# Kernel optimization log

Hardware: AMD Instinct MI355X
Metric: run time of the kernel (lower is better)

The kernel has to match this reference:

```python
import jax, jax.numpy as jnp
import numpy as np

EPS = 1e-5
B, N, M = 4, 256, 256
L, D, INNER = 6, 64, 64  # per-layer output = D//2 = 32 channels


def conv1x1(x, W, b=None):
    # x: [batch, Cin, H, W], W: [Cout, Cin]
    y = jnp.einsum('bchw,oc->bohw', x, W)
    if b is not None:
        y = y + b[None, :, None, None]
    return y


def batchnorm(x, g, b):
    # training-mode BN (default torch .train()): batch stats over (B, H, W)
    mu = x.mean(axis=(0, 2, 3), keepdims=True)
    var = x.var(axis=(0, 2, 3), keepdims=True)
    return g[None, :, None, None] * (x - mu) * jax.lax.rsqrt(var + EPS) + b[None, :, None, None]


def prelu(x, a):
    return jnp.where(x >= 0, x, a * x)


def cross_concat(Z):
    bs = Z.shape[0] // 2
    Za, Zb = Z[:bs], Z[bs:]
    return jnp.concatenate([jnp.concatenate([Za, Zb], 1),
                            jnp.concatenate([Zb, Za], 1)], 0)


def fw_layer(Z, Wm, bm, W, g, be, a):
    # FeatureWeavingLayer with EncoderMaxPool2stream
    bs = Z.shape[0] // 2
    X = cross_concat(Z)                                   # [2bs, 2C, N, M]
    z = conv1x1(X, Wm, bm)                                # [2bs, INNER, N, M]
    za = jnp.broadcast_to(z[:bs].max(axis=2, keepdims=True), z[:bs].shape)
    zb = jnp.broadcast_to(z[bs:].max(axis=3, keepdims=True), z[bs:].shape)
    z = jnp.concatenate([jnp.concatenate([X[:bs], za], 1),
                         jnp.concatenate([X[bs:], zb], 1)], 0)
    z = conv1x1(z, W)                                     # no bias
    z = batchnorm(z, g, be)
    return prelu(z, a)


def weavenet_fwd(Za, Zb, Wm0, bm0, W0, g0, be0, Wm, bm, W, g, be, a, Wf, gf, bf):
    Zb = jnp.swapaxes(Zb, -2, -1)      # [B, C, M, N] -> [B, C, N, M]
    Z = jnp.concatenate([Za, Zb], 0)   # [2B, 1, N, M]
    bs, n, m = Za.shape[0], Za.shape[-2], Za.shape[-1]
    layers = [(Wm0, bm0, W0, g0, be0)] + [(Wm[i], bm[i], W[i], g[i], be[i]) for i in range(L - 1)]
    Z_keep = None
    for i, (Wm_, bm_, W_, g_, be_) in enumerate(layers):
        Z = fw_layer(Z, Wm_, bm_, W_, g_, be_, a)
        if i % 2 == 0:  # use_resnet
            if Z_keep is not None:
                Z = Z + Z_keep
            Z_keep = Z
    Zc = conv1x1(cross_concat(Z), Wf)  # [2B, 1, N, M]
    Zc = batchnorm(Zc, gf, bf)
    m0 = Zc[:bs].reshape(bs, n, m)
    m1 = Zc[bs:].reshape(bs, n, m)
    # HV stream aggregation
    mm = (m0 + m1) / 2.0
    agg = jnp.minimum(jax.nn.softmax(mm, axis=-1), jax.nn.softmax(mm, axis=-2))
    return agg, m0, m1


def setup_inputs() -> dict:
    key = jax.random.key(0)
    ks = jax.random.split(key, 16)
    s = 0.05
    inp = {
        'Za': jax.random.normal(ks[0], (B, 1, N, M), jnp.float32),
        'Zb': jax.random.normal(ks[1], (B, 1, M, N), jnp.float32),
        # layer 0: input_dim = sab_dim*2 = 2
        'Wm0': jax.random.normal(ks[2], (INNER, 2), jnp.float32) * s,
        'bm0': jnp.zeros((INNER,), jnp.float32),
        'W0': jax.random.normal(ks[3], (D // 2, 2 + INNER), jnp.float32) * s,
        'g0': jnp.ones((D // 2,), jnp.float32),
        'be0': jnp.zeros((D // 2,), jnp.float32),
        # layers 1..L-1: input_dim = D = 64
        'Wm': jax.random.normal(ks[4], (L - 1, INNER, D), jnp.float32) * s,
        'bm': jnp.zeros((L - 1, INNER), jnp.float32),
        'W': jax.random.normal(ks[5], (L - 1, D // 2, D + INNER), jnp.float32) * s,
        'g': jnp.ones((L - 1, D // 2), jnp.float32),
        'be': jnp.zeros((L - 1, D // 2), jnp.float32),
        # shared PReLU (single default instance shared across all layers in torch)
        'a': jnp.float32(0.25),
        # final 1x1 conv (in = D after cross_concat) + BN
        'Wf': jax.random.normal(ks[6], (1, D), jnp.float32) * s,
        'gf': jnp.ones((1,), jnp.float32),
        'bf': jnp.zeros((1,), jnp.float32),
    }
    return inp


def reference(Za, Zb, Wm0, bm0, W0, g0, be0, Wm, bm, W, g, be, a, Wf, gf, bf):
    return weavenet_fwd(Za, Zb, Wm0, bm0, W0, g0, be0, Wm, bm, W, g, be, a, Wf, gf, bf)
```

## Files before the change

kernel.cpp:

```cpp
#include <hip/hip_runtime.h>

static constexpr int NMv  = 256;
static constexpr int PIXv = 65536;

__device__ __forceinline__ unsigned fkey(float f){
    unsigned b = __float_as_uint(f);
    return (b & 0x80000000u) ? ~b : (b | 0x80000000u);
}
__device__ __forceinline__ float unfkey(unsigned k){
    unsigned b = (k & 0x80000000u) ? (k & 0x7fffffffu) : ~k;
    return __uint_as_float(b);
}

__global__ __launch_bounds__(256) void k_prep(const float* __restrict__ Za,
                                              const float* __restrict__ Zb,
                                              float* __restrict__ Z){
    __shared__ float tile[32][33];
    int b  = blockIdx.z;
    int tx = threadIdx.x, ty = threadIdx.y;
    int n0 = blockIdx.y * 32, m0 = blockIdx.x * 32;
    if (b < 4){
        const float* src = Za + (size_t)b * PIXv;
        float*       dst = Z  + (size_t)b * PIXv;
        for (int j = 0; j < 32; j += 8){
            int n = n0 + ty + j;
            dst[n * NMv + m0 + tx] = src[n * NMv + m0 + tx];
        }
    } else {
        const float* src = Zb + (size_t)(b - 4) * PIXv;
        for (int j = 0; j < 32; j += 8)
            tile[ty + j][tx] = src[(m0 + ty + j) * NMv + n0 + tx];
        __syncthreads();
        float* dst = Z + (size_t)b * PIXv;
        for (int j = 0; j < 32; j += 8)
            dst[(n0 + ty + j) * NMv + m0 + tx] = tile[tx][ty + j];
    }
}

template<int C>
__global__ __launch_bounds__(256) void k_zmax(const float* __restrict__ Z,
                                              const float* __restrict__ Wm,
                                              const float* __restrict__ bm,
                                              unsigned* __restrict__ zkey){
    constexpr int K2  = 2 * C;
    constexpr int NCH = 8;
    constexpr int NS  = (K2 * 16 + 255) / 256;
    __shared__ float Wms[K2 * 64];
    __shared__ float Xs[K2 * 68];
    int b = blockIdx.z;
    int t = threadIdx.x;
    for (int i = t; i < 64 * K2; i += 256){
        int c = i / K2, k = i % K2;
        Wms[k * 64 + c] = Wm[i];
    }
    const float* Z0 = Z + (size_t)b       * C * PIXv;
    const float* Z1 = Z + (size_t)(b ^ 4) * C * PIXv;
    int m0 = blockIdx.x * 64, n0 = blockIdx.y * NCH;
    int c0 = (t >> 3) * 2, mg = t & 7;
    float bmv0 = bm[c0], bmv1 = bm[c0 + 1];

    float4 rbuf[NS];
    auto issue = [&](int n){
        #pragma unroll
        for (int j = 0; j < NS; j++){
            int s = t + j * 256;
            if (s < K2 * 16){
                int k = s >> 4, m4 = (s & 15) * 4;
                const float* src = (k < C ? Z0 + (size_t)k * PIXv
                                          : Z1 + (size_t)(k - C) * PIXv) + n * NMv + m0 + m4;
                rbuf[j] = *(const float4*)src;
            }
        }
    };
    issue(n0);

    float mx[2][8];
    #pragma unroll
    for (int a = 0; a < 2; a++)
        #pragma unroll
        for (int j = 0; j < 8; j++) mx[a][j] = -3.4e38f;

    for (int ni = 0; ni < NCH; ni++){
        __syncthreads();
        #pragma unroll
        for (int j = 0; j < NS; j++){
            int s = t + j * 256;
            if (s < K2 * 16){
                int k = s >> 4, m4 = (s & 15) * 4;
                *(float4*)&Xs[k * 68 + m4] = rbuf[j];
            }
        }
        if (ni + 1 < NCH) issue(n0 + ni + 1);
        __syncthreads();

        float acc[2][8];
        #pragma unroll
        for (int a = 0; a < 2; a++)
            #pragma unroll
            for (int j = 0; j < 8; j++) acc[a][j] = 0.f;
        #pragma unroll 8
        for (int k = 0; k < K2; k++){
            const float2 w  = *(const float2*)&Wms[k * 64 + c0];
            const float4 x0 = *(const float4*)&Xs[k * 68 + mg * 8];
            const float4 x1 = *(const float4*)&Xs[k * 68 + mg * 8 + 4];
            acc[0][0] += w.x * x0.x; acc[0][1] += w.x * x0.y;
            acc[0][2] += w.x * x0.z; acc[0][3] += w.x * x0.w;
            acc[0][4] += w.x * x1.x; acc[0][5] += w.x * x1.y;
            acc[0][6] += w.x * x1.z; acc[0][7] += w.x * x1.w;
            acc[1][0] += w.y * x0.x; acc[1][1] += w.y * x0.y;
            acc[1][2] += w.y * x0.z; acc[1][3] += w.y * x0.w;
            acc[1][4] += w.y * x1.x; acc[1][5] += w.y * x1.y;
            acc[1][6] += w.y * x1.z; acc[1][7] += w.y * x1.w;
        }

        if (b < 4){
            #pragma unroll
            for (int a = 0; a < 2; a++)
                #pragma unroll
                for (int j = 0; j < 8; j++) mx[a][j] = fmaxf(mx[a][j], acc[a][j]);
        } else {
            int n = n0 + ni;
            #pragma unroll
            for (int a = 0; a < 2; a++){
                float v = fmaxf(fmaxf(fmaxf(acc[a][0], acc[a][1]), fmaxf(acc[a][2], acc[a][3])),
                                fmaxf(fmaxf(acc[a][4], acc[a][5]), fmaxf(acc[a][6], acc[a][7])));
                v = fmaxf(v, __shfl_xor(v, 1));
                v = fmaxf(v, __shfl_xor(v, 2));
                v = fmaxf(v, __shfl_xor(v, 4));
                if (mg == 0)
                    atomicMax(&zkey[((size_t)b * 64 + c0 + a) * NMv + n],
                              fkey(v + (a ? bmv1 : bmv0)));
            }
        }
    }
    if (b < 4){
        #pragma unroll
        for (int a = 0; a < 2; a++){
            float bmv = a ? bmv1 : bmv0;
            #pragma unroll
            for (int j = 0; j < 8; j++)
                atomicMax(&zkey[((size_t)b * 64 + c0 + a) * NMv + m0 + mg * 8 + j],
                          fkey(mx[a][j] + bmv));
        }
    }
}

__global__ __launch_bounds__(256) void k_zmaxw(const unsigned* __restrict__ zkey,
                                               const float* __restrict__ W, int Wst,
                                               float* __restrict__ zmaxW){
    int oc = blockIdx.x, b = blockIdx.y, p = threadIdx.x;
    const float* wrow = W + (size_t)oc * Wst + (Wst - 64);
    float s = 0.f;
    #pragma unroll 8
    for (int c = 0; c < 64; c++)
        s += wrow[c] * unfkey(zkey[((size_t)b * 64 + c) * NMv + p]);
    zmaxW[((size_t)b * 32 + oc) * NMv + p] = s;
}

template<int C>
__global__ __launch_bounds__(256) void k_conv(const float* __restrict__ Z,
                                              const float* __restrict__ Wl,
                                              const float* __restrict__ zmaxW,
                                              float* __restrict__ Y,
                                              float* __restrict__ pstats){
    constexpr int K2 = 2 * C;
    constexpr int KC = (K2 < 16) ? K2 : 16;
    __shared__ float Ws[K2 * 32];
    __shared__ float Xs[KC * 256];
    int b   = blockIdx.y;
    int row = blockIdx.x;
    int t   = threadIdx.x;
    int p4  = t & 63, og = t >> 6;
    for (int i = t; i < K2 * 32; i += 256){
        int k = i >> 5, oc = i & 31;
        Ws[i] = Wl[(size_t)oc * (K2 + 64) + k];
    }
    const float* Z0 = Z + ((size_t)b       * C) * PIXv + (size_t)row * NMv;
    const float* Z1 = Z + ((size_t)(b ^ 4) * C) * PIXv + (size_t)row * NMv;
    float acc[4][8];
    #pragma unroll
    for (int j = 0; j < 4; j++)
        #pragma unroll
        for (int o = 0; o < 8; o++) acc[j][o] = 0.f;

    for (int kc = 0; kc < K2; kc += KC){
        __syncthreads();
        for (int s = t; s < KC * 64; s += 256){
            int k = kc + (s >> 6), m4 = (s & 63) * 4;
            const float* src = (k < C ? Z0 + (size_t)k * PIXv
                                      : Z1 + (size_t)(k - C) * PIXv) + m4;
            *(float4*)&Xs[(s >> 6) * 256 + m4] = *(const float4*)src;
        }
        __syncthreads();
        #pragma unroll 4
        for (int kk = 0; kk < KC; kk++){
            const float4 xv = *(const float4*)&Xs[kk * 256 + p4 * 4];
            const float4 wa = *(const float4*)&Ws[(kc + kk) * 32 + og * 8];
            const float4 wb = *(const float4*)&Ws[(kc + kk) * 32 + og * 8 + 4];
            const float xx[4] = {xv.x, xv.y, xv.z, xv.w};
            const float ww[8] = {wa.x, wa.y, wa.z, wa.w, wb.x, wb.y, wb.z, wb.w};
            #pragma unroll
            for (int j = 0; j < 4; j++)
                #pragma unroll
                for (int o = 0; o < 8; o++)
                    acc[j][o] += xx[j] * ww[o];
        }
    }
    if (b < 4){
        #pragma unroll
        for (int o = 0; o < 8; o++){
            float4 zw = *(const float4*)&zmaxW[((size_t)b * 32 + og * 8 + o) * NMv + p4 * 4];
            acc[0][o] += zw.x; acc[1][o] += zw.y; acc[2][o] += zw.z; acc[3][o] += zw.w;
        }
    } else {
        #pragma unroll
        for (int o = 0; o < 8; o++){
            float zw = zmaxW[((size_t)b * 32 + og * 8 + o) * NMv + row];
            acc[0][o] += zw; acc[1][o] += zw; acc[2][o] += zw; acc[3][o] += zw;
        }
    }
    float* yb = Y + ((size_t)b * 32 + og * 8) * PIXv + (size_t)row * NMv + p4 * 4;
    #pragma unroll
    for (int o = 0; o < 8; o++){
        float4 v = make_float4(acc[0][o], acc[1][o], acc[2][o], acc[3][o]);
        *(float4*)(yb + (size_t)o * PIXv) = v;
    }
    int blk = b * 256 + row;
    #pragma unroll
    for (int o = 0; o < 8; o++){
        float s1 = acc[0][o] + acc[1][o] + acc[2][o] + acc[3][o];
        float s2 = acc[0][o] * acc[0][o] + acc[1][o] * acc[1][o] +
                   acc[2][o] * acc[2][o] + acc[3][o] * acc[3][o];
        #pragma unroll
        for (int d = 32; d > 0; d >>= 1){
            s1 += __shfl_down(s1, d);
            s2 += __shfl_down(s2, d);
        }
        if ((t & 63) == 0){
            int c = og * 8 + o;
            pstats[(size_t)c        * 2048 + blk] = s1;
            pstats[(size_t)(32 + c) * 2048 + blk] = s2;
        }
    }
}

__global__ __launch_bounds__(256) void k_reduce(const float* __restrict__ src,
                                                float* __restrict__ dst){
    __shared__ float ls[4];
    int row = blockIdx.x, t = threadIdx.x;
    const float* p = src + (size_t)row * 2048 + t;
    float s = 0.f;
    #pragma unroll
    for (int j = 0; j < 8; j++) s += p[j * 256];
    #pragma unroll
    for (int d = 32; d > 0; d >>= 1) s += __shfl_down(s, d);
    if ((t & 63) == 0) ls[t >> 6] = s;
    __syncthreads();
    if (t == 0) dst[row] = ls[0] + ls[1] + ls[2] + ls[3];
}

__global__ __launch_bounds__(256) void k_bnapply(const float* __restrict__ Y,
                                                 const float* __restrict__ stats,
                                                 const float* __restrict__ g,
                                                 const float* __restrict__ be,
                                                 const float* __restrict__ keep_in,
                                                 const float* __restrict__ aptr,
                                                 float* __restrict__ Zout,
                                                 float* __restrict__ keep_out){
    __shared__ float s_sc[32], s_sh[32];
    if (threadIdx.x < 32){
        int c = threadIdx.x;
        const float inv = 1.f / (8.f * PIXv);
        float mu  = stats[c] * inv;
        float var = stats[32 + c] * inv - mu * mu;
        float sc  = g[c] * rsqrtf(var + 1e-5f);
        s_sc[c] = sc;
        s_sh[c] = be[c] - mu * sc;
    }
    __syncthreads();
    const float al = *aptr;
    const size_t tot = (size_t)8 * 32 * PIXv / 4;
    for (size_t i = (size_t)blockIdx.x * 256 + threadIdx.x; i < tot;
         i += (size_t)gridDim.x * 256){
        int c = (int)((i >> 14) & 31);
        float4 y = ((const float4*)Y)[i];
        float sc = s_sc[c], sh = s_sh[c];
        float4 v;
        v.x = sc * y.x + sh; v.y = sc * y.y + sh;
        v.z = sc * y.z + sh; v.w = sc * y.w + sh;
        v.x = v.x >= 0.f ? v.x : al * v.x;
        v.y = v.y >= 0.f ? v.y : al * v.y;
        v.z = v.z >= 0.f ? v.z : al * v.z;
        v.w = v.w >= 0.f ? v.w : al * v.w;
        if (keep_in){
            float4 kz = ((const float4*)keep_in)[i];
            v.x += kz.x; v.y += kz.y; v.z += kz.z; v.w += kz.w;
        }
        ((float4*)Zout)[i] = v;
        if (keep_out) ((float4*)keep_out)[i] = v;
    }
}

__global__ __launch_bounds__(256) void k_final(const float* __restrict__ Z,
                                               const float* __restrict__ Wf,
                                               float* __restrict__ T,
                                               float* __restrict__ pfin){
    int b = blockIdx.y;
    size_t base = (size_t)blockIdx.x * 1024 + (size_t)threadIdx.x * 4;
    const float* Z0 = Z + (size_t)b       * 32 * PIXv + base;
    const float* Z1 = Z + (size_t)(b ^ 4) * 32 * PIXv + base;
    float4 acc = make_float4(0.f, 0.f, 0.f, 0.f);
    #pragma unroll 8
    for (int c = 0; c < 32; c++){
        float w0 = Wf[c], w1 = Wf[32 + c];
        float4 x0 = *(const float4*)(Z0 + (size_t)c * PIXv);
        float4 x1 = *(const float4*)(Z1 + (size_t)c * PIXv);
        acc.x += w0 * x0.x + w1 * x1.x;
        acc.y += w0 * x0.y + w1 * x1.y;
        acc.z += w0 * x0.z + w1 * x1.z;
        acc.w += w0 * x0.w + w1 * x1.w;
    }
    *(float4*)(T + (size_t)b * PIXv + base) = acc;
    float a1 = acc.x + acc.y + acc.z + acc.w;
    float a2 = acc.x * acc.x + acc.y * acc.y + acc.z * acc.z + acc.w * acc.w;
    #pragma unroll
    for (int d = 32; d > 0; d >>= 1){
        a1 += __shfl_down(a1, d);
        a2 += __shfl_down(a2, d);
    }
    if ((threadIdx.x & 63) == 0){
        int slot = (blockIdx.y * 64 + blockIdx.x) * 4 + (threadIdx.x >> 6);
        pfin[slot]        = a1;
        pfin[2048 + slot] = a2;
    }
}

__global__ __launch_bounds__(256) void k_mm(const float* __restrict__ T,
                                            const float* __restrict__ fstats,
                                            const float* __restrict__ gf,
                                            const float* __restrict__ bf,
                                            float* __restrict__ out,
                                            float* __restrict__ MMb){
    const float inv = 1.f / (8.f * PIXv);
    float mu  = fstats[0] * inv;
    float var = fstats[1] * inv - mu * mu;
    float sc  = gf[0] * rsqrtf(var + 1e-5f);
    float sh  = bf[0] - mu * sc;
    size_t e = ((size_t)blockIdx.x * 256 + threadIdx.x) * 4;
    float4 t0 = *(const float4*)(T + e);
    float4 t1 = *(const float4*)(T + (size_t)4 * PIXv + e);
    float4 m0, m1, mv;
    m0.x = sc * t0.x + sh; m0.y = sc * t0.y + sh; m0.z = sc * t0.z + sh; m0.w = sc * t0.w + sh;
    m1.x = sc * t1.x + sh; m1.y = sc * t1.y + sh; m1.z = sc * t1.z + sh; m1.w = sc * t1.w + sh;
    mv.x = 0.5f * (m0.x + m1.x); mv.y = 0.5f * (m0.y + m1.y);
    mv.z = 0.5f * (m0.z + m1.z); mv.w = 0.5f * (m0.w + m1.w);
    *(float4*)(out + (size_t)4 * PIXv + e) = m0;
    *(float4*)(out + (size_t)8 * PIXv + e) = m1;
    *(float4*)(MMb + e) = mv;
}

__global__ __launch_bounds__(256) void k_rowstats(const float* __restrict__ MMb,
                                                  float* __restrict__ rmax,
                                                  float* __restrict__ rsum){
    int wid = threadIdx.x >> 6, lane = threadIdx.x & 63;
    int r = blockIdx.x * 4 + wid;
    const float* p = MMb + (size_t)r * NMv;
    float4 v = *(const float4*)(p + lane * 4);
    float mx = fmaxf(fmaxf(v.x, v.y), fmaxf(v.z, v.w));
    #pragma unroll
    for (int d = 32; d > 0; d >>= 1) mx = fmaxf(mx, __shfl_xor(mx, d));
    float s = expf(v.x - mx) + expf(v.y - mx) + expf(v.z - mx) + expf(v.w - mx);
    #pragma unroll
    for (int d = 32; d > 0; d >>= 1) s += __shfl_xor(s, d);
    if (lane == 0){ rmax[r] = mx; rsum[r] = s; }
}

__global__ __launch_bounds__(256) void k_colmax(const float* __restrict__ MMb,
                                                unsigned* __restrict__ ckey){
    int b = blockIdx.y, ch = blockIdx.x, m = threadIdx.x;
    const float* p = MMb + (size_t)b * PIXv + (size_t)ch * 16 * NMv + m;
    float mx = -3.4e38f;
    #pragma unroll
    for (int n = 0; n < 16; n++) mx = fmaxf(mx, p[(size_t)n * NMv]);
    atomicMax(&ckey[b * NMv + m], fkey(mx));
}
__global__ __launch_bounds__(256) void k_colsum(const float* __restrict__ MMb,
                                                const unsigned* __restrict__ ckey,
                                                float* __restrict__ csum){
    int b = blockIdx.y, ch = blockIdx.x, m = threadIdx.x;
    const float* p = MMb + (size_t)b * PIXv + (size_t)ch * 16 * NMv + m;
    float cm = unfkey(ckey[b * NMv + m]);
    float s = 0.f;
    #pragma unroll
    for (int n = 0; n < 16; n++) s += expf(p[(size_t)n * NMv] - cm);
    atomicAdd(&csum[b * NMv + m], s);
}

__global__ __launch_bounds__(256) void k_agg(const float* __restrict__ MMb,
                                             const float* __restrict__ rmax,
                                             const float* __restrict__ rsum,
                                             const unsigned* __restrict__ ckey,
                                             const float* __restrict__ csum,
                                             float* __restrict__ out){
    size_t e = ((size_t)blockIdx.x * 256 + threadIdx.x) * 4;
    int r = (int)(e >> 8);
    int b = (int)(e >> 16);
    int m = (int)(e & 255);
    int cb = b * NMv + m;
    float rm = rmax[r], rsi = 1.f / rsum[r];
    float4 v = *(const float4*)(MMb + e);
    float4 o;
    o.x = fminf(expf(v.x - rm) * rsi, expf(v.x - unfkey(ckey[cb + 0])) / csum[cb + 0]);
    o.y = fminf(expf(v.y - rm) * rsi, expf(v.y - unfkey(ckey[cb + 1])) / csum[cb + 1]);
    o.z = fminf(expf(v.z - rm) * rsi, expf(v.z - unfkey(ckey[cb + 2])) / csum[cb + 2]);
    o.w = fminf(expf(v.w - rm) * rsi, expf(v.w - unfkey(ckey[cb + 3])) / csum[cb + 3]);
    *(float4*)(out + e) = o;
}

extern "C" void kernel_launch(void* const* d_in, const int* in_sizes, int n_in,
                              void* d_out, int out_size, void* d_ws, size_t ws_size,
                              hipStream_t stream){
    (void)in_sizes; (void)n_in; (void)out_size; (void)ws_size;
    const float* Za  = (const float*)d_in[0];
    const float* Zb  = (const float*)d_in[1];
    const float* Wm0 = (const float*)d_in[2];
    const float* bm0 = (const float*)d_in[3];
    const float* W0  = (const float*)d_in[4];
    const float* g0  = (const float*)d_in[5];
    const float* be0 = (const float*)d_in[6];
    const float* Wm  = (const float*)d_in[7];
    const float* bm  = (const float*)d_in[8];
    const float* W   = (const float*)d_in[9];
    const float* g   = (const float*)d_in[10];
    const float* be  = (const float*)d_in[11];
    const float* ap  = (const float*)d_in[12];
    const float* Wf  = (const float*)d_in[13];
    const float* gf  = (const float*)d_in[14];
    const float* bf  = (const float*)d_in[15];
    float* out = (float*)d_out;

    size_t off = 0;
    char* wsb = (char*)d_ws;
    auto alloc = [&](size_t bytes) -> void* {
        void* p = wsb + off;
        off += (bytes + 255) & ~(size_t)255;
        return p;
    };
    float*    Zbuf  = (float*)   alloc((size_t)8 * 32 * PIXv * 4);
    float*    Zkeep = (float*)   alloc((size_t)8 * 32 * PIXv * 4);
    float*    Ybuf  = (float*)   alloc((size_t)8 * 32 * PIXv * 4);
    unsigned* zkey  = (unsigned*)alloc((size_t)8 * 64 * NMv * 4);
    float*    zmaxW = (float*)   alloc((size_t)8 * 32 * NMv * 4);
    float*    stats = (float*)   alloc(64 * 4);
    float*    T     = (float*)   alloc((size_t)8 * PIXv * 4);
    float*    fstats= (float*)   alloc(2 * 4);
    float*    MMb   = (float*)   alloc((size_t)4 * PIXv * 4);
    float*    rmaxb = (float*)   alloc(1024 * 4);
    float*    rsumb = (float*)   alloc(1024 * 4);
    unsigned* ckey  = (unsigned*)alloc(1024 * 4);
    float*    csum  = (float*)   alloc(1024 * 4);
    float*    pstats= (float*)   alloc((size_t)64 * 2048 * 4);
    float*    pfin  = (float*)   alloc((size_t)2 * 2048 * 4);

    k_prep<<<dim3(8, 8, 8), dim3(32, 8), 0, stream>>>(Za, Zb, Zbuf);

    for (int i = 0; i < 6; i++){
        const float *Wm_l, *bm_l, *W_l, *g_l, *be_l;
        int C;
        if (i == 0){ Wm_l = Wm0; bm_l = bm0; W_l = W0; g_l = g0; be_l = be0; C = 1; }
        else {
            Wm_l = Wm + (size_t)(i - 1) * 64 * 64;
            bm_l = bm + (size_t)(i - 1) * 64;
            W_l  = W  + (size_t)(i - 1) * 32 * 128;
            g_l  = g  + (size_t)(i - 1) * 32;
            be_l = be + (size_t)(i - 1) * 32;
            C = 32;
        }
        hipMemsetAsync(zkey, 0, (size_t)8 * 64 * NMv * 4, stream);
        if (C == 1) k_zmax<1 ><<<dim3(4, 32, 8), 256, 0, stream>>>(Zbuf, Wm_l, bm_l, zkey);
        else        k_zmax<32><<<dim3(4, 32, 8), 256, 0, stream>>>(Zbuf, Wm_l, bm_l, zkey);
        k_zmaxw<<<dim3(32, 8), 256, 0, stream>>>(zkey, W_l, 2 * C + 64, zmaxW);
        if (C == 1) k_conv<1 ><<<dim3(256, 8), 256, 0, stream>>>(Zbuf, W_l, zmaxW, Ybuf, pstats);
        else        k_conv<32><<<dim3(256, 8), 256, 0, stream>>>(Zbuf, W_l, zmaxW, Ybuf, pstats);
        k_reduce<<<64, 256, 0, stream>>>(pstats, stats);
        bool addk   = (i == 2 || i == 4);
        bool storek = (i % 2 == 0);
        k_bnapply<<<4096, 256, 0, stream>>>(Ybuf, stats, g_l, be_l,
                                            addk ? Zkeep : (const float*)nullptr, ap,
                                            Zbuf, storek ? Zkeep : (float*)nullptr);
    }

    k_final<<<dim3(64, 8), 256, 0, stream>>>(Zbuf, Wf, T, pfin);
    k_reduce<<<2, 256, 0, stream>>>(pfin, fstats);
    k_mm<<<256, 256, 0, stream>>>(T, fstats, gf, bf, out, MMb);
    k_rowstats<<<256, 256, 0, stream>>>(MMb, rmaxb, rsumb);
    hipMemsetAsync(ckey, 0, 1024 * 4, stream);
    hipMemsetAsync(csum, 0, 1024 * 4, stream);
    k_colmax<<<dim3(16, 4), 256, 0, stream>>>(MMb, ckey);
    k_colsum<<<dim3(16, 4), 256, 0, stream>>>(MMb, ckey, csum);
    k_agg<<<256, 256, 0, stream>>>(MMb, rmaxb, rsumb, ckey, csum, out);
}
```

Before: 1.340 ms.

## Replace atomicMax reductions in zmax with partial buffers and a reduce kernel

The zmax kernel no longer does atomicMax on order-preserving integer keys. It writes per-block partial maxima into scratch space borrowed from Ybuf, and a new k_zred kernel reduces them and adds the bias. This removes the atomic traffic and the per-layer memset. The kernel is also re-tiled so each thread computes 4 channels and each block handles two rows per iteration, giving more register reuse. The cost is an extra kernel launch and extra partial-buffer traffic, because pzA holds 64 partials per channel.

```diff
diff --git a/kernel.cpp b/kernel.cpp
--- a/kernel.cpp
+++ b/kernel.cpp
@@ -40,13 +40,15 @@
 template<int C>
 __global__ __launch_bounds__(256) void k_zmax(const float* __restrict__ Z,
                                               const float* __restrict__ Wm,
-                                              const float* __restrict__ bm,
-                                              unsigned* __restrict__ zkey){
-    constexpr int K2  = 2 * C;
-    constexpr int NCH = 8;
-    constexpr int NS  = (K2 * 16 + 255) / 256;
+                                              float* __restrict__ pzA,
+                                              float* __restrict__ pzB){
+    constexpr int K2    = 2 * C;
+    constexpr int NITER = 4;
+    constexpr int PRS   = K2 * 16;
+    constexpr int SLOTS = 2 * PRS;
+    constexpr int NS    = (SLOTS + 255) / 256;
     __shared__ float Wms[K2 * 64];
-    __shared__ float Xs[K2 * 68];
+    __shared__ float Xs[2 * K2 * 68];
     int b = blockIdx.z;
     int t = threadIdx.x;
     for (int i = t; i < 64 * K2; i += 256){
@@ -55,97 +57,115 @@
     }
     const float* Z0 = Z + (size_t)b       * C * PIXv;
     const float* Z1 = Z + (size_t)(b ^ 4) * C * PIXv;
-    int m0 = blockIdx.x * 64, n0 = blockIdx.y * NCH;
-    int c0 = (t >> 3) * 2, mg = t & 7;
-    float bmv0 = bm[c0], bmv1 = bm[c0 + 1];
+    int m0 = blockIdx.x * 64, n0 = blockIdx.y * (2 * NITER);
+    int row_sel = t >> 7, tid = t & 127;
+    int c0 = (tid >> 3) * 4, mg = tid & 7;
 
     float4 rbuf[NS];
-    auto issue = [&](int n){
+    auto issue = [&](int base){
         #pragma unroll
         for (int j = 0; j < NS; j++){
             int s = t + j * 256;
-            if (s < K2 * 16){
-                int k = s >> 4, m4 = (s & 15) * 4;
+            if (s < SLOTS){
+                int row = s / PRS, r = s % PRS, k = r >> 4, m4 = r & 15;
                 const float* src = (k < C ? Z0 + (size_t)k * PIXv
-                                          : Z1 + (size_t)(k - C) * PIXv) + n * NMv + m0 + m4;
+                                          : Z1 + (size_t)(k - C) * PIXv)
+                                   + (n0 + base + row) * NMv + m0 + m4 * 4;
                 rbuf[j] = *(const float4*)src;
             }
         }
     };
-    issue(n0);
-
-    float mx[2][8];
-    #pragma unroll
-    for (int a = 0; a < 2; a++)
+    issue(0);
+
+    float mx[4][8];
+    #pragma unroll
+    for (int a = 0; a < 4; a++)
         #pragma unroll
         for (int j = 0; j < 8; j++) mx[a][j] = -3.4e38f;
 
-    for (int ni = 0; ni < NCH; ni++){
+    for (int it = 0; it < NITER; ++it){
         __syncthreads();
         #pragma unroll
         for (int j = 0; j < NS; j++){
             int s = t + j * 256;
-            if (s < K2 * 16){
-                int k = s >> 4, m4 = (s & 15) * 4;
-                *(float4*)&Xs[k * 68 + m4] = rbuf[j];
+            if (s < SLOTS){
+                int row = s / PRS, r = s % PRS, k = r >> 4, m4 = r & 15;
+                *(float4*)&Xs[row * (K2 * 68) + k * 68 + m4 * 4] = rbuf[j];
             }
         }
-        if (ni + 1 < NCH) issue(n0 + ni + 1);
+        if (it + 1 < NITER) issue(2 * (it + 1));
         __syncthreads();
 
-        float acc[2][8];
-        #pragma unroll
-        for (int a = 0; a < 2; a++)
+        float acc[4][8];
+        #pragma unroll
+        for (int a = 0; a < 4; a++)
             #pragma unroll
             for (int j = 0; j < 8; j++) acc[a][j] = 0.f;
+        const float* Xr = &Xs[row_sel * (K2 * 68)];
         #pragma unroll 8
         for (int k = 0; k < K2; k++){
-            const float2 w  = *(const float2*)&Wms[k * 64 + c0];
-            const float4 x0 = *(const float4*)&Xs[k * 68 + mg * 8];
-            const float4 x1 = *(const float4*)&Xs[k * 68 + mg * 8 + 4];
-            acc[0][0] += w.x * x0.x; acc[0][1] += w.x * x0.y;
-            acc[0][2] += w.x * x0.z; acc[0][3] += w.x * x0.w;
-            acc[0][4] += w.x * x1.x; acc[0][5] += w.x * x1.y;
-            acc[0][6] += w.x * x1.z; acc[0][7] += w.x * x1.w;
-            acc[1][0] += w.y * x0.x; acc[1][1] += w.y * x0.y;
-            acc[1][2] += w.y * x0.z; acc[1][3] += w.y * x0.w;
-            acc[1][4] += w.y * x1.x; acc[1][5] += w.y * x1.y;
-            acc[1][6] += w.y * x1.z; acc[1][7] += w.y * x1.w;
+            const float4 w  = *(const float4*)&Wms[k * 64 + c0];
+            const float4 x0 = *(const float4*)&Xr[k * 68 + mg * 8];
+            const float4 x1 = *(const float4*)&Xr[k * 68 + mg * 8 + 4];
+            const float wv[4] = {w.x, w.y, w.z, w.w};
+            const float xv[8] = {x0.x, x0.y, x0.z, x0.w, x1.x, x1.y, x1.z, x1.w};
+            #pragma unroll
+            for (int a = 0; a < 4; a++)
+                #pragma unroll
+                for (int j = 0; j < 8; j++)
+                    acc[a][j] += wv[a] * xv[j];
         }
 
         if (b < 4){
             #pragma unroll
-            for (int a = 0; a < 2; a++)
+            for (int a = 0; a < 4; a++)
                 #pragma unroll
                 for (int j = 0; j < 8; j++) mx[a][j] = fmaxf(mx[a][j], acc[a][j]);
         } else {
-            int n = n0 + ni;
+            int n = n0 + 2 * it + row_sel;
             #pragma unroll
-            for (int a = 0; a < 2; a++){
+            for (int a = 0; a < 4; a++){
                 float v = fmaxf(fmaxf(fmaxf(acc[a][0], acc[a][1]), fmaxf(acc[a][2], acc[a][3])),
                                 fmaxf(fmaxf(acc[a][4], acc[a][5]), fmaxf(acc[a][6], acc[a][7])));
                 v = fmaxf(v, __shfl_xor(v, 1));
                 v = fmaxf(v, __shfl_xor(v, 2));
                 v = fmaxf(v, __shfl_xor(v, 4));
                 if (mg == 0)
-                    atomicMax(&zkey[((size_t)b * 64 + c0 + a) * NMv + n],
-                              fkey(v + (a ? bmv1 : bmv0)));
+                    pzB[(((size_t)(b - 4) * 64 + c0 + a) * NMv + n) * 4 + blockIdx.x] = v;
             }
         }
     }
     if (b < 4){
-        #pragma unroll
-        for (int a = 0; a < 2; a++){
-            float bmv = a ? bmv1 : bmv0;
-            #pragma unroll
-            for (int j = 0; j < 8; j++)
-                atomicMax(&zkey[((size_t)b * 64 + c0 + a) * NMv + m0 + mg * 8 + j],
-                          fkey(mx[a][j] + bmv));
-        }
-    }
-}
-
-__global__ __launch_bounds__(256) void k_zmaxw(const unsigned* __restrict__ zkey,
+        int ch2 = blockIdx.y * 2 + row_sel;
+        #pragma unroll
+        for (int a = 0; a < 4; a++){
+            float* dst = &pzA[(((size_t)b * 64 + ch2) * 64 + c0 + a) * NMv + m0 + mg * 8];
+            *(float4*)dst       = make_float4(mx[a][0], mx[a][1], mx[a][2], mx[a][3]);
+            *(float4*)(dst + 4) = make_float4(mx[a][4], mx[a][5], mx[a][6], mx[a][7]);
+        }
+    }
+}
+
+__global__ __launch_bounds__(256) void k_zred(const float* __restrict__ pzA,
+                                              const float* __restrict__ pzB,
+                                              const float* __restrict__ bm,
+                                              float* __restrict__ zmaxf){
+    int c = blockIdx.x, b = blockIdx.y, p = threadIdx.x;
+    float v;
+    if (b < 4){
+        v = -3.4e38f;
+        const float* src = pzA + ((size_t)b * 64 * 64 + c) * NMv + p;
+        #pragma unroll 8
+        for (int j = 0; j < 64; j++)
+            v = fmaxf(v, src[(size_t)j * 64 * NMv]);
+    } else {
+        const float4 q = *(const float4*)&pzB[(((size_t)(b - 4) * 64 + c) * NMv + p) * 4];
+        v = fmaxf(fmaxf(q.x, q.y), fmaxf(q.z, q.w));
+    }
+    zmaxf[((size_t)b * 64 + c) * NMv + p] = v + bm[c];
+}
+
+__global__ __launch_bounds__(256) void k_zmaxw(const float* __restrict__ zmaxf,
                                                const float* __restrict__ W, int Wst,
                                                float* __restrict__ zmaxW){
     int oc = blockIdx.x, b = blockIdx.y, p = threadIdx.x;
@@ -153,7 +173,7 @@
     float s = 0.f;
     #pragma unroll 8
     for (int c = 0; c < 64; c++)
-        s += wrow[c] * unfkey(zkey[((size_t)b * 64 + c) * NMv + p]);
+        s += wrow[c] * zmaxf[((size_t)b * 64 + c) * NMv + p];
     zmaxW[((size_t)b * 32 + oc) * NMv + p] = s;
 }
 
@@ -449,7 +469,7 @@
     float*    Zbuf  = (float*)   alloc((size_t)8 * 32 * PIXv * 4);
     float*    Zkeep = (float*)   alloc((size_t)8 * 32 * PIXv * 4);
     float*    Ybuf  = (float*)   alloc((size_t)8 * 32 * PIXv * 4);
-    unsigned* zkey  = (unsigned*)alloc((size_t)8 * 64 * NMv * 4);
+    float*    zmaxf = (float*)   alloc((size_t)8 * 64 * NMv * 4);
     float*    zmaxW = (float*)   alloc((size_t)8 * 32 * NMv * 4);
     float*    stats = (float*)   alloc(64 * 4);
     float*    T     = (float*)   alloc((size_t)8 * PIXv * 4);
@@ -462,6 +482,9 @@
     float*    pstats= (float*)   alloc((size_t)64 * 2048 * 4);
     float*    pfin  = (float*)   alloc((size_t)2 * 2048 * 4);
 
+    float* pzA = Ybuf;
+    float* pzB = Ybuf + (size_t)4 * 64 * 64 * NMv;
+
     k_prep<<<dim3(8, 8, 8), dim3(32, 8), 0, stream>>>(Za, Zb, Zbuf);
 
     for (int i = 0; i < 6; i++){
@@ -476,10 +499,10 @@
             be_l = be + (size_t)(i - 1) * 32;
             C = 32;
         }
-        hipMemsetAsync(zkey, 0, (size_t)8 * 64 * NMv * 4, stream);
-        if (C == 1) k_zmax<1 ><<<dim3(4, 32, 8), 256, 0, stream>>>(Zbuf, Wm_l, bm_l, zkey);
-        else        k_zmax<32><<<dim3(4, 32, 8), 256, 0, stream>>>(Zbuf, Wm_l, bm_l, zkey);
-        k_zmaxw<<<dim3(32, 8), 256, 0, stream>>>(zkey, W_l, 2 * C + 64, zmaxW);
+        if (C == 1) k_zmax<1 ><<<dim3(4, 32, 8), 256, 0, stream>>>(Zbuf, Wm_l, pzA, pzB);
+        else        k_zmax<32><<<dim3(4, 32, 8), 256, 0, stream>>>(Zbuf, Wm_l, pzA, pzB);
+        k_zred<<<dim3(64, 8), 256, 0, stream>>>(pzA, pzB, bm_l, zmaxf);
+        k_zmaxw<<<dim3(32, 8), 256, 0, stream>>>(zmaxf, W_l, 2 * C + 64, zmaxW);
         if (C == 1) k_conv<1 ><<<dim3(256, 8), 256, 0, stream>>>(Zbuf, W_l, zmaxW, Ybuf, pstats);
         else        k_conv<32><<<dim3(256, 8), 256, 0, stream>>>(Zbuf, W_l, zmaxW, Ybuf, pstats);
         k_reduce<<<64, 256, 0, stream>>>(pstats, stats);
```

After: 1.162 ms. -13.3%, faster.
